# Kernel optimization log

Hardware: AMD Instinct MI355X
Metric: run time of the kernel (lower is better)

The kernel has to match this reference:

```python
import jax, jax.numpy as jnp
import numpy as np

NUM_HEADS = 16


def sinusoidal_pe(N, C, dtype=jnp.float32):
    # matches the numpy construction in get_positional_encoding
    pos = jnp.arange(N, dtype=dtype)[:, None]                  # [N,1]
    dims = jnp.arange(C)                                        # [C]
    rates = 1.0 / jnp.power(jnp.asarray(10000.0, dtype), (2 * (dims // 2)).astype(dtype) / C)
    ang = pos * rates                                           # [N,C]
    pe = jnp.where(dims % 2 == 0, jnp.sin(ang), jnp.cos(ang))
    return pe.astype(dtype)


def setup_inputs() -> dict:
    key = jax.random.key(0)
    k1, k2, k3 = jax.random.split(key, 3)
    B, N, C = 4, 2048, 1024
    inputs = jax.random.normal(k1, (B, N, C), dtype=jnp.float32)
    mask_mat = jax.random.uniform(k2, (B, N), dtype=jnp.float32)
    # Glorot-uniform qkv kernel [C, 3C]
    limit = float(np.sqrt(6.0 / (C + 3 * C)))
    W_qkv = jax.random.uniform(k3, (C, 3 * C), dtype=jnp.float32, minval=-limit, maxval=limit)
    return {"inputs": inputs, "mask_mat": mask_mat, "W_qkv": W_qkv}


def reference(inputs, mask_mat, W_qkv):
    B, N, C = inputs.shape
    H = NUM_HEADS
    hd = C // H
    scale = hd ** (-0.5)

    # additive mask: -(m outer m), broadcast over heads
    neg_mask = -(mask_mat[:, :, None] * mask_mat[:, None, :])   # [B,N,N]

    x = inputs + sinusoidal_pe(N, C, inputs.dtype)              # APE
    qkv = jnp.einsum('bnc,cd->bnd', x, W_qkv)                   # [B,N,3C]
    qkv = qkv.reshape(B, N, 3, H, hd).transpose(2, 0, 3, 1, 4)  # [3,B,H,N,hd]
    q, k, v = qkv[0], qkv[1], qkv[2]

    attn = jnp.einsum('bhnd,bhmd->bhnm', q, k) * scale          # [B,H,N,N]
    attn = attn + neg_mask[:, None, :, :]
    attn = jax.nn.softmax(attn, axis=-1)
    out = jnp.einsum('bhnm,bhmd->bhnd', attn, v)                # [B,H,N,hd]
    return out.transpose(0, 2, 1, 3).reshape(B, N, C)
```

## Files before the change

kernel.cpp:

```cpp
#include <hip/hip_runtime.h>
#include <hip/hip_bf16.h>

typedef unsigned short u16;
typedef __bf16 bf16x8 __attribute__((ext_vector_type(8)));
typedef float floatx4 __attribute__((ext_vector_type(4)));

#define B_ 4
#define N_ 2048
#define C_ 1024
#define H_ 16
#define HD_ 64

__device__ __forceinline__ float b2f(u16 u) {
    union { float f; unsigned int i; } v; v.i = ((unsigned int)u) << 16; return v.f;
}
__device__ __forceinline__ u16 f2b(float f) {
    union { float f; unsigned int i; } v; v.f = f;
    unsigned int i = v.i;
    unsigned int r = i + 0x7FFFu + ((i >> 16) & 1u);
    return (u16)(r >> 16);
}
__device__ __forceinline__ unsigned int pk2(float a, float b) {
    __hip_bfloat162 t = __float22bfloat162_rn(float2{a, b});
    unsigned int u; __builtin_memcpy(&u, &t, 4); return u;
}
__device__ __forceinline__ float fexp2(float x) {
    return __builtin_amdgcn_exp2f(x);
}
__device__ __forceinline__ void async16(const u16* g, u16* l) {
    __builtin_amdgcn_global_load_lds((const __attribute__((address_space(1))) unsigned int*)g,
                                     (__attribute__((address_space(3))) unsigned int*)l,
                                     16, 0, 0);
}
__device__ __forceinline__ void async16p(const void* g, void* l) {
    __builtin_amdgcn_global_load_lds((const __attribute__((address_space(1))) unsigned int*)g,
                                     (__attribute__((address_space(3))) unsigned int*)l,
                                     16, 0, 0);
}

__global__ __launch_bounds__(256) void pe_add_kernel(const float* __restrict__ in,
                                                     u16* __restrict__ x) {
    int idx = blockIdx.x * 256 + threadIdx.x;
    int cp  = idx & 511;
    int row = idx >> 9;
    int n   = row & (N_ - 1);
    float r = exp2f(-13.287712379549449f * ((float)cp * (1.0f / 512.0f)));
    float ang = (float)n * r;
    float s, c;
    sincosf(ang, &s, &c);
    float2 pr = ((const float2*)in)[idx];
    unsigned int o = ((unsigned int)f2b(pr.y + c) << 16) | (unsigned int)f2b(pr.x + s);
    ((unsigned int*)x)[idx] = o;
}

__global__ __launch_bounds__(256) void wt_kernel(const float* __restrict__ W,
                                                 u16* __restrict__ Wt) {
    __shared__ u16 tile[32][33];
    int bx = blockIdx.x;
    int by = blockIdx.y;
    int tx = threadIdx.x & 31;
    int ty = threadIdx.x >> 5;
    for (int i = 0; i < 32; i += 8)
        tile[ty + i][tx] = f2b(W[(size_t)(by * 32 + ty + i) * 3072 + bx * 32 + tx]);
    __syncthreads();
    for (int i = 0; i < 32; i += 8)
        Wt[(size_t)(bx * 32 + ty + i) * 1024 + by * 32 + tx] = tile[tx][ty + i];
}

__global__ __launch_bounds__(256) void qkv_gemm_kernel(const u16* __restrict__ X,
                                                       const u16* __restrict__ Wt,
                                                       u16* __restrict__ q,
                                                       u16* __restrict__ k,
                                                       u16* __restrict__ vt) {
    __shared__ u16 As[128 * 64];
    __shared__ u16 Bs[128 * 64];
    int tid  = threadIdx.x;
    int wave = tid >> 6, lane = tid & 63, l15 = lane & 15, quad = lane >> 4;
    int m0 = blockIdx.x * 128;
    int n0 = blockIdx.y * 128;
    int wm = (wave & 1) * 64;
    int wn = (wave >> 1) * 64;

    floatx4 acc[4][4];
    for (int i = 0; i < 4; i++)
        for (int j = 0; j < 4; j++)
            acc[i][j] = floatx4{0.f, 0.f, 0.f, 0.f};

    int rowOff = wave * 32 + (lane >> 3);
    int colSw  = ((lane & 7) ^ (lane >> 3)) * 8;
    const u16* gA = X  + (size_t)(m0 + rowOff) * 1024 + colSw;
    const u16* gB = Wt + (size_t)(n0 + rowOff) * 1024 + colSw;
    u16* lA = As + wave * 2048;
    u16* lB = Bs + wave * 2048;

    int swl = l15 & 7;
    int aB0 = (wm + l15) * 64 + ((quad ^ swl) * 8);
    int aB1 = (wm + l15) * 64 + (((4 + quad) ^ swl) * 8);
    int bB0 = (wn + l15) * 64 + ((quad ^ swl) * 8);
    int bB1 = (wn + l15) * 64 + (((4 + quad) ^ swl) * 8);

    for (int k0 = 0; k0 < 1024; k0 += 64) {
        __syncthreads();
        async16(gA + k0,             lA);
        async16(gA + k0 +  8 * 1024, lA + 512);
        async16(gA + k0 + 16 * 1024, lA + 1024);
        async16(gA + k0 + 24 * 1024, lA + 1536);
        async16(gB + k0,             lB);
        async16(gB + k0 +  8 * 1024, lB + 512);
        async16(gB + k0 + 16 * 1024, lB + 1024);
        async16(gB + k0 + 24 * 1024, lB + 1536);
        __syncthreads();

        bf16x8 af[4][2], bf[4][2];
        for (int i = 0; i < 4; i++) {
            af[i][0] = *(const bf16x8*)(As + aB0 + i * 16 * 64);
            af[i][1] = *(const bf16x8*)(As + aB1 + i * 16 * 64);
        }
        for (int j = 0; j < 4; j++) {
            bf[j][0] = *(const bf16x8*)(Bs + bB0 + j * 16 * 64);
            bf[j][1] = *(const bf16x8*)(Bs + bB1 + j * 16 * 64);
        }
        for (int i = 0; i < 4; i++)
            for (int j = 0; j < 4; j++) {
                acc[i][j] = __builtin_amdgcn_mfma_f32_16x16x32_bf16(af[i][0], bf[j][0], acc[i][j], 0, 0, 0);
                acc[i][j] = __builtin_amdgcn_mfma_f32_16x16x32_bf16(af[i][1], bf[j][1], acc[i][j], 0, 0, 0);
            }
    }

    const float QSC = 0.125f * 1.44269504f;
    for (int i = 0; i < 4; i++) {
        int gm   = m0 + wm + i * 16 + quad * 4;
        int b    = gm >> 11;
        int nloc = gm & 2047;
        for (int j = 0; j < 4; j++) {
            int gn    = n0 + wn + j * 16 + l15;
            int which = gn >> 10;
            int cc    = gn & 1023;
            int h     = cc >> 6;
            int d     = cc & 63;
            size_t bh = (size_t)(b * 16 + h);
            if (which == 2) {
                ushort4 w4;
                w4.x = f2b(acc[i][j][0]);
                w4.y = f2b(acc[i][j][1]);
                w4.z = f2b(acc[i][j][2]);
                w4.w = f2b(acc[i][j][3]);
                *(ushort4*)(vt + (bh * 64 + d) * 2048 + nloc) = w4;
            } else {
                u16* dst = (which == 0) ? q : k;
                float sc = (which == 0) ? QSC : 1.0f;
                for (int r = 0; r < 4; r++)
                    dst[(bh * 2048 + nloc + r) * 64 + d] = f2b(acc[i][j][r] * sc);
            }
        }
    }
}

__global__ __launch_bounds__(256, 4) void attn_kernel(const u16* __restrict__ q,
                                                      const u16* __restrict__ k,
                                                      const u16* __restrict__ vt,
                                                      const float* __restrict__ mask,
                                                      float* __restrict__ out) {
    __shared__ u16 Ks[3][32 * 64];
    __shared__ u16 Vs[3][64 * 32];
    __shared__ u16 Ps[4][32 * 40];
    __shared__ __align__(16) float Msr[3][256];

    int tid  = threadIdx.x;
    int wave = tid >> 6, lane = tid & 63, l15 = lane & 15, quad = lane >> 4;
    int bid = blockIdx.x;
    int bh = bid & 63, qb = bid >> 6;
    int b = bh >> 4, h = bh & 15;
    size_t base = (size_t)bh * (N_ * 64);
    int q0 = qb * 128 + wave * 32;
    const float* mkb = mask + b * N_;

    bf16x8 qf[2][2];
#pragma unroll
    for (int s = 0; s < 2; s++)
#pragma unroll
        for (int dc = 0; dc < 2; dc++)
            qf[s][dc] = *(const bf16x8*)(q + base + (size_t)(q0 + s * 16 + l15) * 64 + dc * 32 + quad * 8);

    const float L2E = 1.44269504f;
    float nmq[2];
    nmq[0] = -L2E * mkb[q0 + l15];
    nmq[1] = -L2E * mkb[q0 + 16 + l15];

    bf16x8 onef;
#pragma unroll
    for (int i = 0; i < 8; i++) onef[i] = (__bf16)1.0f;

    floatx4 acc[2][4];
    floatx4 accl[2];
#pragma unroll
    for (int s = 0; s < 2; s++) {
        accl[s] = floatx4{0.f, 0.f, 0.f, 0.f};
#pragma unroll
        for (int dt = 0; dt < 4; dt++)
            acc[s][dt] = floatx4{0.f, 0.f, 0.f, 0.f};
    }

    int krow = wave * 8  + (lane >> 3);
    int kcol = ((lane & 7) ^ (lane >> 3)) * 8;
    int vrow = wave * 16 + (lane >> 2);
    int vcol = ((lane & 3) ^ ((lane >> 2) & 3)) * 8;
    const u16* gK = k  + base + (size_t)krow * 64 + kcol;
    const u16* gV = vt + ((size_t)bh * 64 + vrow) * 2048 + vcol;
    const float* gM = mkb + (lane & 7) * 4;
    int wof = wave * 512;

    int a0 = ((quad    ) ^ (l15 & 7)) * 8;
    int a1 = ((4 + quad) ^ (l15 & 7)) * 8;
    int av = ( quad      ^ (l15 & 3)) * 8;

    u16* Pw = Ps[wave];

    auto TILE = [&](int kt, const u16* Kb, const u16* Vb, const float* Mb,
                    u16* Kn, u16* Vn, float* Mn) {
        asm volatile("s_waitcnt vmcnt(3)" ::: "memory");
        __builtin_amdgcn_s_barrier();
        __builtin_amdgcn_sched_barrier(0);
        int nkt = kt + 64; if (nkt > N_ - 32) nkt = N_ - 32;
        async16(gK + (size_t)nkt * 64, Kn);
        async16(gV + nkt,              Vn);
        async16p(gM + nkt,             Mn);
        float4 mkv0 = *(const float4*)(Mb + quad * 4);
        float4 mkv1 = *(const float4*)(Mb + 16 + quad * 4);
#pragma unroll
        for (int t = 0; t < 2; t++) {
            bf16x8 kf0 = *(const bf16x8*)(Kb + (t * 16 + l15) * 64 + a0);
            bf16x8 kf1 = *(const bf16x8*)(Kb + (t * 16 + l15) * 64 + a1);
            float4 mk = t ? mkv1 : mkv0;
#pragma unroll
            for (int s = 0; s < 2; s++) {
                floatx4 sa;
                sa[0] = nmq[s] * mk.x;
                sa[1] = nmq[s] * mk.y;
                sa[2] = nmq[s] * mk.z;
                sa[3] = nmq[s] * mk.w;
                __builtin_amdgcn_s_setprio(1);
                sa = __builtin_amdgcn_mfma_f32_16x16x32_bf16(kf0, qf[s][0], sa, 0, 0, 0);
                sa = __builtin_amdgcn_mfma_f32_16x16x32_bf16(kf1, qf[s][1], sa, 0, 0, 0);
                __builtin_amdgcn_s_setprio(0);
                float p0 = fexp2(sa[0]);
                float p1 = fexp2(sa[1]);
                float p2 = fexp2(sa[2]);
                float p3 = fexp2(sa[3]);
                uint2 w; w.x = pk2(p0, p1); w.y = pk2(p2, p3);
                *(uint2*)(Pw + (s * 16 + l15) * 40 + t * 16 + quad * 4) = w;
            }
        }
        bf16x8 pf0 = *(const bf16x8*)(Pw + l15 * 40 + quad * 8);
        bf16x8 pf1 = *(const bf16x8*)(Pw + (16 + l15) * 40 + quad * 8);
        __builtin_amdgcn_s_setprio(1);
        accl[0] = __builtin_amdgcn_mfma_f32_16x16x32_bf16(pf0, onef, accl[0], 0, 0, 0);
        accl[1] = __builtin_amdgcn_mfma_f32_16x16x32_bf16(pf1, onef, accl[1], 0, 0, 0);
        __builtin_amdgcn_s_setprio(0);
#pragma unroll
        for (int dt = 0; dt < 4; dt++) {
            bf16x8 vf = *(const bf16x8*)(Vb + (dt * 16 + l15) * 32 + av);
            __builtin_amdgcn_s_setprio(1);
            acc[0][dt] = __builtin_amdgcn_mfma_f32_16x16x32_bf16(pf0, vf, acc[0][dt], 0, 0, 0);
            acc[1][dt] = __builtin_amdgcn_mfma_f32_16x16x32_bf16(pf1, vf, acc[1][dt], 0, 0, 0);
            __builtin_amdgcn_s_setprio(0);
        }
    };

    asm volatile("s_waitcnt vmcnt(0)" ::: "memory");
    async16(gK,            Ks[0] + wof);
    async16(gV,            Vs[0] + wof);
    async16p(gM,           Msr[0]);
    async16(gK + 32 * 64,  Ks[1] + wof);
    async16(gV + 32,       Vs[1] + wof);
    async16p(gM + 32,      Msr[1]);
    __syncthreads();

    for (int m = 0; m < 21; ++m) {
        int kt = m * 96;
        TILE(kt,      Ks[0], Vs[0], Msr[0], Ks[2] + wof, Vs[2] + wof, Msr[2]);
        TILE(kt + 32, Ks[1], Vs[1], Msr[1], Ks[0] + wof, Vs[0] + wof, Msr[0]);
        TILE(kt + 64, Ks[2], Vs[2], Msr[2], Ks[1] + wof, Vs[1] + wof, Msr[1]);
    }
    TILE(2016, Ks[0], Vs[0], Msr[0], Ks[2] + wof, Vs[2] + wof, Msr[2]);

#pragma unroll
    for (int s = 0; s < 2; s++) {
#pragma unroll
        for (int r = 0; r < 4; r++) {
            float ir = 1.0f / accl[s][r];
            int qrow = q0 + s * 16 + quad * 4 + r;
            float* orow = out + ((size_t)(b * N_ + qrow)) * C_ + h * 64;
#pragma unroll
            for (int dt = 0; dt < 4; dt++)
                orow[dt * 16 + l15] = acc[s][dt][r] * ir;
        }
    }
}

extern "C" void kernel_launch(void* const* d_in, const int* in_sizes, int n_in,
                              void* d_out, int out_size, void* d_ws, size_t ws_size,
                              hipStream_t stream) {
    const float* inp  = (const float*)d_in[0];
    const float* mask = (const float*)d_in[1];
    const float* W    = (const float*)d_in[2];
    float* out = (float*)d_out;

    char* ws = (char*)d_ws;
    u16* x  = (u16*)ws;
    u16* Wt = (u16*)(ws + 16777216);
    u16* q  = (u16*)(ws + 23068672);
    u16* k  = q + 8388608;
    u16* vt = k + 8388608;

    pe_add_kernel<<<16384, 256, 0, stream>>>(inp, x);
    wt_kernel<<<dim3(96, 32), 256, 0, stream>>>(W, Wt);
    qkv_gemm_kernel<<<dim3(64, 24), 256, 0, stream>>>(x, Wt, q, k, vt);
    attn_kernel<<<1024, 256, 0, stream>>>(q, k, vt, mask, out);
}
```

Before: 242.8 us.

## Keep softmax probabilities in registers instead of round-tripping through LDS

The exponentiated scores are now packed straight into the MFMA A-operand registers, replacing the write to a per-wave LDS P buffer and the read back. The K-dimension ordering of P is permuted to match the S accumulator layout, and the V fragment is gathered from two 8-byte LDS reads at matching offsets so the P·V contraction stays consistent. The conversion uses the hardware v_cvt_pk_bf16_f32 instruction through inline asm. This removes LDS traffic and a shared buffer, which may raise occupancy, at the cost of twice as many narrower V loads.

```diff
diff --git a/kernel.cpp b/kernel.cpp
--- a/kernel.cpp
+++ b/kernel.cpp
@@ -20,12 +20,13 @@
     unsigned int r = i + 0x7FFFu + ((i >> 16) & 1u);
     return (u16)(r >> 16);
 }
-__device__ __forceinline__ unsigned int pk2(float a, float b) {
-    __hip_bfloat162 t = __float22bfloat162_rn(float2{a, b});
-    unsigned int u; __builtin_memcpy(&u, &t, 4); return u;
-}
 __device__ __forceinline__ float fexp2(float x) {
     return __builtin_amdgcn_exp2f(x);
+}
+__device__ __forceinline__ unsigned int pkraw(float a, float b) {
+    unsigned int u;
+    asm("v_cvt_pk_bf16_f32 %0, %1, %2" : "=v"(u) : "v"(a), "v"(b));
+    return u;
 }
 __device__ __forceinline__ void async16(const u16* g, u16* l) {
     __builtin_amdgcn_global_load_lds((const __attribute__((address_space(1))) unsigned int*)g,
@@ -163,7 +164,6 @@
                                                       float* __restrict__ out) {
     __shared__ u16 Ks[3][32 * 64];
     __shared__ u16 Vs[3][64 * 32];
-    __shared__ u16 Ps[4][32 * 40];
     __shared__ __align__(16) float Msr[3][256];
 
     int tid  = threadIdx.x;
@@ -212,9 +212,8 @@
 
     int a0 = ((quad    ) ^ (l15 & 7)) * 8;
     int a1 = ((4 + quad) ^ (l15 & 7)) * 8;
-    int av = ( quad      ^ (l15 & 3)) * 8;
-
-    u16* Pw = Ps[wave];
+    int o1 = (((quad >> 1)    ) ^ (l15 & 3)) * 8 + (quad & 1) * 4;
+    int o2 = (((quad >> 1) + 2) ^ (l15 & 3)) * 8 + (quad & 1) * 4;
 
     auto TILE = [&](int kt, const u16* Kb, const u16* Vb, const float* Mb,
                     u16* Kn, u16* Vn, float* Mn) {
@@ -227,6 +226,7 @@
         async16p(gM + nkt,             Mn);
         float4 mkv0 = *(const float4*)(Mb + quad * 4);
         float4 mkv1 = *(const float4*)(Mb + 16 + quad * 4);
+        float p[2][2][4];
 #pragma unroll
         for (int t = 0; t < 2; t++) {
             bf16x8 kf0 = *(const bf16x8*)(Kb + (t * 16 + l15) * 64 + a0);
@@ -243,26 +243,36 @@
                 sa = __builtin_amdgcn_mfma_f32_16x16x32_bf16(kf0, qf[s][0], sa, 0, 0, 0);
                 sa = __builtin_amdgcn_mfma_f32_16x16x32_bf16(kf1, qf[s][1], sa, 0, 0, 0);
                 __builtin_amdgcn_s_setprio(0);
-                float p0 = fexp2(sa[0]);
-                float p1 = fexp2(sa[1]);
-                float p2 = fexp2(sa[2]);
-                float p3 = fexp2(sa[3]);
-                uint2 w; w.x = pk2(p0, p1); w.y = pk2(p2, p3);
-                *(uint2*)(Pw + (s * 16 + l15) * 40 + t * 16 + quad * 4) = w;
+                p[s][t][0] = fexp2(sa[0]);
+                p[s][t][1] = fexp2(sa[1]);
+                p[s][t][2] = fexp2(sa[2]);
+                p[s][t][3] = fexp2(sa[3]);
             }
         }
-        bf16x8 pf0 = *(const bf16x8*)(Pw + l15 * 40 + quad * 8);
-        bf16x8 pf1 = *(const bf16x8*)(Pw + (16 + l15) * 40 + quad * 8);
+        bf16x8 pf[2];
+#pragma unroll
+        for (int s = 0; s < 2; s++) {
+            uint4 u;
+            u.x = pkraw(p[s][0][0], p[s][0][1]);
+            u.y = pkraw(p[s][0][2], p[s][0][3]);
+            u.z = pkraw(p[s][1][0], p[s][1][1]);
+            u.w = pkraw(p[s][1][2], p[s][1][3]);
+            __builtin_memcpy(&pf[s], &u, 16);
+        }
         __builtin_amdgcn_s_setprio(1);
-        accl[0] = __builtin_amdgcn_mfma_f32_16x16x32_bf16(pf0, onef, accl[0], 0, 0, 0);
-        accl[1] = __builtin_amdgcn_mfma_f32_16x16x32_bf16(pf1, onef, accl[1], 0, 0, 0);
+        accl[0] = __builtin_amdgcn_mfma_f32_16x16x32_bf16(pf[0], onef, accl[0], 0, 0, 0);
+        accl[1] = __builtin_amdgcn_mfma_f32_16x16x32_bf16(pf[1], onef, accl[1], 0, 0, 0);
         __builtin_amdgcn_s_setprio(0);
 #pragma unroll
         for (int dt = 0; dt < 4; dt++) {
-            bf16x8 vf = *(const bf16x8*)(Vb + (dt * 16 + l15) * 32 + av);
+            const u16* vr = Vb + (dt * 16 + l15) * 32;
+            uint2 v1 = *(const uint2*)(vr + o1);
+            uint2 v2 = *(const uint2*)(vr + o2);
+            uint4 vv; vv.x = v1.x; vv.y = v1.y; vv.z = v2.x; vv.w = v2.y;
+            bf16x8 vf; __builtin_memcpy(&vf, &vv, 16);
             __builtin_amdgcn_s_setprio(1);
-            acc[0][dt] = __builtin_amdgcn_mfma_f32_16x16x32_bf16(pf0, vf, acc[0][dt], 0, 0, 0);
-            acc[1][dt] = __builtin_amdgcn_mfma_f32_16x16x32_bf16(pf1, vf, acc[1][dt], 0, 0, 0);
+            acc[0][dt] = __builtin_amdgcn_mfma_f32_16x16x32_bf16(pf[0], vf, acc[0][dt], 0, 0, 0);
+            acc[1][dt] = __builtin_amdgcn_mfma_f32_16x16x32_bf16(pf[1], vf, acc[1][dt], 0, 0, 0);
             __builtin_amdgcn_s_setprio(0);
         }
     };
```

Measured after the change: 232.2 us. 1.05x faster.
